# Optimization experiments

Measured on AMD Instinct MI355X. Metric: run time of the kernel, lower is better.

The kernel has to match this reference:

```python
import jax, jax.numpy as jnp
import numpy as np

N = 4096   # num_nodes
D_E = 16   # node embedding dim
H = 4      # heads
K = 3      # Chebyshev order
L = 64     # in_dim
B = 16     # batch


def setup_inputs() -> dict:
    key = jax.random.key(0)
    ks = jax.random.split(key, 8)
    return {
        "x": jax.random.normal(ks[0], (B, N, L), dtype=jnp.float32),
        "psi_emb": jax.random.normal(ks[1], (N, D_E), dtype=jnp.float32),
        "psi": jnp.asarray(1.0, dtype=jnp.float32),
        "W_q": jax.random.normal(ks[2], (D_E, H, D_E), dtype=jnp.float32),
        "W_k": jax.random.normal(ks[3], (D_E, H, D_E), dtype=jnp.float32),
        "attn_alpha": jnp.asarray(0.5, dtype=jnp.float32),
        "F_w": jax.random.normal(ks[4], (H, D_E, K + 1, L), dtype=jnp.float32),
        "f_b": jax.random.normal(ks[5], (H, D_E), dtype=jnp.float32),
        "head_mix": jnp.ones((H,), dtype=jnp.float32),
    }


def reference(x, psi_emb, psi, W_q, W_k, attn_alpha, F_w, f_b, head_mix):
    # x: (B, N, L) -> out: (B, N)
    Bx, Nx, Lx = x.shape

    # Gaussian adjacency: softmax over rows of exp(-psi * ||psi_i - psi_j||^2)
    diff = psi_emb[:, None, :] - psi_emb[None, :, :]      # (N, N, d_e)
    dist2 = jnp.sum(diff * diff, axis=-1)                 # (N, N)
    A_g = jax.nn.softmax(jnp.exp(-psi * dist2), axis=1)   # (N, N)

    # Per-head attention adjacency
    Q = jnp.einsum('nd,dhm->nhm', psi_emb, W_q)           # (N, H, d_e)
    Kt = jnp.einsum('nd,dhm->nhm', psi_emb, W_k)          # (N, H, d_e)
    scale = 1.0 / np.sqrt(Q.shape[-1]).astype(np.float32)
    attn = jnp.einsum('nhd,mhd->hnm', Q, Kt) * scale      # (H, N, N)
    A_attn = jax.nn.softmax(attn, axis=-1)

    # Sigmoid blend of gaussian and attention adjacencies
    alpha = jax.nn.sigmoid(attn_alpha)
    A_effs = alpha * A_g[None, :, :] + (1.0 - alpha) * A_attn  # (H, N, N)

    mix_w = jax.nn.softmax(head_mix)                      # (H,)
    I = jnp.eye(Nx, dtype=x.dtype)

    out = jnp.zeros((Bx, Nx), dtype=x.dtype)
    for h in range(H):  # small fixed head loop (structurally distinct params)
        A = A_effs[h]
        # Chebyshev recursion: T0=I, T1=A, Tk = 2 A T_{k-1} - T_{k-2}
        supports = [I, A]
        for _ in range(2, K + 1):
            supports.append(2.0 * (A @ supports[-1]) - supports[-2])
        S = jnp.stack(supports, axis=0)                   # (K+1, N, N)

        # Per-node filter weights / bias from node embeddings
        W_filter = jnp.einsum('nd,dkl->nkl', psi_emb, F_w[h])  # (N, K+1, L)
        b_filter = psi_emb @ f_b[h]                            # (N,)

        x_g = jnp.einsum('knm,bml->bknl', S, x)                # (B, K+1, N, L)
        out_h = jnp.einsum('bknl,nkl->bn', x_g, W_filter) + b_filter
        out = out + mix_w[h] * out_h
    return out
```

## Files before the change

kernel.cpp:

```cpp
#include <hip/hip_runtime.h>
#include <hip/hip_bf16.h>

#define NN 4096
#define DE 16
#define NH 4
#define LL 64
#define NB 16
#define CC 1024

typedef __attribute__((ext_vector_type(8))) short short8v;
typedef __attribute__((ext_vector_type(4))) float f32x4;

#define GLD_LDS16(gp, lp) __builtin_amdgcn_global_load_lds( \
    (const __attribute__((address_space(1))) unsigned int*)(gp), \
    (__attribute__((address_space(3))) unsigned int*)(lp), 16, 0, 0)

__device__ __forceinline__ unsigned short f2bf(float f){
  unsigned int u = __float_as_uint(f);
  u += 0x7fffu + ((u >> 16) & 1u);
  return (unsigned short)(u >> 16);
}
__device__ __forceinline__ float bf2f(unsigned short s){
  return __uint_as_float(((unsigned int)s) << 16);
}
__device__ __forceinline__ void get_mix(const float* hm, float* mw){
  float a=hm[0],b=hm[1],c=hm[2],d=hm[3];
  float m = fmaxf(fmaxf(a,b),fmaxf(c,d));
  float e0=__expf(a-m),e1=__expf(b-m),e2=__expf(c-m),e3=__expf(d-m);
  float inv = 1.0f/(e0+e1+e2+e3);
  mw[0]=e0*inv; mw[1]=e1*inv; mw[2]=e2*inv; mw[3]=e3*inv;
}

__global__ void k_prep(const float* __restrict__ psi_emb, const float* __restrict__ W_q,
                       const float* __restrict__ W_k, const float* __restrict__ f_b,
                       const float* __restrict__ head_mix,
                       unsigned short* __restrict__ Qh, unsigned short* __restrict__ Ql,
                       unsigned short* __restrict__ Kh, unsigned short* __restrict__ Kl,
                       unsigned short* __restrict__ Ph, unsigned short* __restrict__ Pl,
                       float* __restrict__ n2g, float* __restrict__ bias_comb){
  int n = blockIdx.x*blockDim.x + threadIdx.x;
  if (n >= NN) return;
  float p[DE];
  float n2 = 0.f;
  unsigned short ph[DE], pl[DE];
  #pragma unroll
  for (int d=0;d<DE;d++){
    p[d] = psi_emb[n*DE+d];
    n2 += p[d]*p[d];
    ph[d] = f2bf(p[d]);
    pl[d] = f2bf(p[d] - bf2f(ph[d]));
  }
  n2g[n] = n2;
  *(short8v*)(Ph + n*DE)     = *(short8v*)ph;
  *(short8v*)(Ph + n*DE + 8) = *(short8v*)(ph+8);
  *(short8v*)(Pl + n*DE)     = *(short8v*)pl;
  *(short8v*)(Pl + n*DE + 8) = *(short8v*)(pl+8);
  float mw[NH]; get_mix(head_mix, mw);
  float bias = 0.f;
  for (int h=0; h<NH; h++){
    unsigned short qh[DE], ql[DE], kh[DE], kl[DE];
    #pragma unroll
    for (int m=0;m<DE;m++){
      float q=0.f,k=0.f;
      #pragma unroll
      for (int d=0;d<DE;d++){
        q += p[d]*W_q[(d*NH+h)*DE+m];
        k += p[d]*W_k[(d*NH+h)*DE+m];
      }
      qh[m]=f2bf(q); ql[m]=f2bf(q - bf2f(qh[m]));
      kh[m]=f2bf(k); kl[m]=f2bf(k - bf2f(kh[m]));
    }
    size_t base = ((size_t)h*NN + n)*DE;
    *(short8v*)(Qh+base)=*(short8v*)qh;   *(short8v*)(Qh+base+8)=*(short8v*)(qh+8);
    *(short8v*)(Ql+base)=*(short8v*)ql;   *(short8v*)(Ql+base+8)=*(short8v*)(ql+8);
    *(short8v*)(Kh+base)=*(short8v*)kh;   *(short8v*)(Kh+base+8)=*(short8v*)(kh+8);
    *(short8v*)(Kl+base)=*(short8v*)kl;   *(short8v*)(Kl+base+8)=*(short8v*)(kl+8);
    float bh=0.f;
    #pragma unroll
    for (int d=0;d<DE;d++) bh += p[d]*f_b[h*DE+d];
    bias += mw[h]*bh;
  }
  bias_comb[n]=bias;
}

__global__ void k_wf(const float* __restrict__ psi_emb, const float* __restrict__ F_w,
                     const float* __restrict__ head_mix,
                     float* __restrict__ Wf_eff, float* __restrict__ W0c){
  int id = blockIdx.x*256 + threadIdx.x;
  int n = id & (NN-1);
  int kl = id >> 12;
  int l = kl & (LL-1);
  int k = kl >> 6;
  float mw[NH]; get_mix(head_mix, mw);
  float p[DE];
  #pragma unroll
  for (int d=0;d<DE;d++) p[d]=psi_emb[n*DE+d];
  float s0=0.f;
  for (int h=0;h<NH;h++){
    float v=0.f;
    #pragma unroll
    for (int d=0;d<DE;d++) v += p[d]*F_w[((h*DE+d)*4+k)*LL+l];
    v *= mw[h];
    Wf_eff[(((size_t)(h*4+k))*LL+l)*NN+n]=v;
    s0 += v;
  }
  if (k==0) W0c[(size_t)l*NN+n]=s0;
}

__global__ __launch_bounds__(256, 4) void k_adj(
    const unsigned short* __restrict__ Qh, const unsigned short* __restrict__ Ql,
    const unsigned short* __restrict__ Kh, const unsigned short* __restrict__ Kl,
    const unsigned short* __restrict__ Ph, const unsigned short* __restrict__ Pl,
    const float* __restrict__ n2g, const float* __restrict__ psi_p,
    const float* __restrict__ attn_alpha, unsigned short* __restrict__ A_all){
  __shared__ unsigned short T[4][16][72];
  __shared__ float st_g[4][16], st_m[4][16], st_s[4][16];
  __shared__ float fin_g[16], fin_m[16], fin_s[16];

  int tid = threadIdx.x;
  int lane = tid & 63, w = tid >> 6;
  int h = blockIdx.y;
  int n0 = blockIdx.x * 16;
  int kg = lane >> 4;
  int cl = lane & 15;
  float psi_v = psi_p[0];
  float alpha = 1.f/(1.f+__expf(-attn_alpha[0]));

  short8v z8 = {};
  int rown = n0 + cl;
  const unsigned short* qb = ((kg<2) ? Qh : Ql) + ((size_t)h*NN + rown)*DE + (kg&1)*8;
  const unsigned short* pb = ((kg<2) ? Ph : Pl) + (size_t)rown*DE + (kg&1)*8;
  short8v aF1 = *(const short8v*)qb;
  short8v gA1 = *(const short8v*)pb;
  short8v aF2 = z8, gA2 = z8;
  if (kg < 2){ aF2 = aF1; gA2 = gA1; }

  float n2row[4];
  #pragma unroll
  for (int r=0;r<4;r++) n2row[r] = n2g[n0 + kg*4 + r];

  float gsum[4], mx[4], sm[4];
  #pragma unroll
  for (int r=0;r<4;r++){ gsum[r]=0.f; mx[r]=-1e30f; sm[r]=0.f; }

  const size_t hN = (size_t)h*NN;
  int mbase = w * 1024;

  #pragma unroll 2
  for (int mt=0; mt<64; ++mt){
    int m0 = mbase + mt*16;
    int mm = m0 + cl;
    const unsigned short* kb = Kh + (hN + mm)*DE + (kg&1)*8;
    const unsigned short* pmb = Ph + (size_t)mm*DE + (kg&1)*8;
    short8v bF1 = *(const short8v*)kb;
    short8v gB1 = *(const short8v*)pmb;
    short8v bF2 = z8, gB2 = z8;
    if (kg < 2){
      bF2 = *(const short8v*)(Kl + (hN + mm)*DE + (kg&1)*8);
      gB2 = *(const short8v*)(Pl + (size_t)mm*DE + (kg&1)*8);
    }
    f32x4 zc = {};
    f32x4 sc = __builtin_amdgcn_mfma_f32_16x16x32_bf16(aF2, bF2, zc, 0,0,0);
    sc = __builtin_amdgcn_mfma_f32_16x16x32_bf16(aF1, bF1, sc, 0,0,0);
    f32x4 gc = __builtin_amdgcn_mfma_f32_16x16x32_bf16(gA2, gB2, zc, 0,0,0);
    gc = __builtin_amdgcn_mfma_f32_16x16x32_bf16(gA1, gB1, gc, 0,0,0);
    float n2m = n2g[m0 + cl];
    #pragma unroll
    for (int r=0;r<4;r++){
      float s = sc[r]*0.25f;
      float d2 = n2row[r] + n2m - 2.f*gc[r];
      float eg = __expf(__expf(-psi_v*d2));
      gsum[r] += eg;
      if (s > mx[r] + 8.f){
        sm[r] = sm[r]*__expf(mx[r]-s) + 1.f;
        mx[r] = s;
      } else {
        sm[r] += __expf(s - mx[r]);
      }
    }
  }
  #pragma unroll
  for (int off=1; off<16; off<<=1){
    #pragma unroll
    for (int r=0;r<4;r++){
      gsum[r] += __shfl_xor(gsum[r], off);
      float om = __shfl_xor(mx[r], off);
      float os = __shfl_xor(sm[r], off);
      float nm = fmaxf(mx[r], om);
      sm[r] = sm[r]*__expf(mx[r]-nm) + os*__expf(om-nm);
      mx[r] = nm;
    }
  }
  if (cl < 4){
    float g,m,s;
    if      (cl==0){ g=gsum[0]; m=mx[0]; s=sm[0]; }
    else if (cl==1){ g=gsum[1]; m=mx[1]; s=sm[1]; }
    else if (cl==2){ g=gsum[2]; m=mx[2]; s=sm[2]; }
    else           { g=gsum[3]; m=mx[3]; s=sm[3]; }
    int row = kg*4 + cl;
    st_g[w][row]=g; st_m[w][row]=m; st_s[w][row]=s;
  }
  __syncthreads();
  if (tid < 16){
    float G=0.f, M=-1e30f, S=0.f;
    #pragma unroll
    for (int ww=0; ww<4; ww++){
      G += st_g[ww][tid];
      float om = st_m[ww][tid], os = st_s[ww][tid];
      float nm = fmaxf(M, om);
      S = S*__expf(M-nm) + os*__expf(om-nm);
      M = nm;
    }
    fin_g[tid] = 1.f/G;
    fin_m[tid] = M;
    fin_s[tid] = 1.f/S;
  }
  __syncthreads();

  float fg[4], fm[4], fs[4];
  #pragma unroll
  for (int r=0;r<4;r++){
    fg[r]=fin_g[kg*4+r]; fm[r]=fin_m[kg*4+r]; fs[r]=fin_s[kg*4+r];
  }
  float a1 = alpha, a2 = 1.f - alpha;

  for (int mt=0; mt<64; ++mt){
    int m0 = mbase + mt*16;
    int mm = m0 + cl;
    const unsigned short* kb = Kh + (hN + mm)*DE + (kg&1)*8;
    const unsigned short* pmb = Ph + (size_t)mm*DE + (kg&1)*8;
    short8v bF1 = *(const short8v*)kb;
    short8v gB1 = *(const short8v*)pmb;
    short8v bF2 = z8, gB2 = z8;
    if (kg < 2){
      bF2 = *(const short8v*)(Kl + (hN + mm)*DE + (kg&1)*8);
      gB2 = *(const short8v*)(Pl + (size_t)mm*DE + (kg&1)*8);
    }
    f32x4 zc = {};
    f32x4 sc = __builtin_amdgcn_mfma_f32_16x16x32_bf16(aF2, bF2, zc, 0,0,0);
    sc = __builtin_amdgcn_mfma_f32_16x16x32_bf16(aF1, bF1, sc, 0,0,0);
    f32x4 gc = __builtin_amdgcn_mfma_f32_16x16x32_bf16(gA2, gB2, zc, 0,0,0);
    gc = __builtin_amdgcn_mfma_f32_16x16x32_bf16(gA1, gB1, gc, 0,0,0);
    float n2m = n2g[m0 + cl];
    #pragma unroll
    for (int r=0;r<4;r++){
      float s = sc[r]*0.25f;
      float d2 = n2row[r] + n2m - 2.f*gc[r];
      float eg = __expf(__expf(-psi_v*d2));
      float ag  = eg * fg[r];
      float aat = __expf(s - fm[r]) * fs[r];
      float a = a1*ag + a2*aat;
      T[w][kg*4+r][(mt&3)*16 + cl] = f2bf(a);
    }
    if ((mt & 3) == 3){
      int row = lane >> 2, cgp = lane & 3;
      short8v v0 = *(const short8v*)&T[w][row][cgp*16];
      short8v v1 = *(const short8v*)&T[w][row][cgp*16+8];
      unsigned short* dst = A_all + hN*NN + (size_t)(n0+row)*NN + mbase + (mt&~3)*16 + cgp*16;
      *(short8v*)dst = v0;
      *(short8v*)(dst+8) = v1;
    }
  }
}

__global__ __launch_bounds__(256) void k_xpose(const float* __restrict__ x,
                                               unsigned short* __restrict__ X){
  __shared__ float t[64][65];
  int b = blockIdx.y, n0 = blockIdx.x*64;
  int tid=threadIdx.x;
  int nr = tid>>2, lc=(tid&3)*16;
  const float* src = x + ((size_t)b*NN + n0 + nr)*LL + lc;
  #pragma unroll
  for (int j=0;j<16;j+=4){
    float4 v = *(const float4*)(src + j);
    t[nr][lc+j+0]=v.x; t[nr][lc+j+1]=v.y; t[nr][lc+j+2]=v.z; t[nr][lc+j+3]=v.w;
  }
  __syncthreads();
  int cl = tid>>2, mp=(tid&3)*16;
  short8v bufv[2];
  #pragma unroll
  for (int j=0;j<16;j++) bufv[j>>3][j&7] = (short)f2bf(t[mp+j][cl]);
  unsigned short* dst = X + (size_t)(b*LL+cl)*NN + n0 + mp;
  *(short8v*)dst = bufv[0];
  *(short8v*)(dst+8) = bufv[1];
}

__global__ void k_out0(const float* __restrict__ x, const float* __restrict__ W0c,
                       const float* __restrict__ bias_comb, float* __restrict__ out){
  int id = blockIdx.x*256+threadIdx.x;
  int n = id & (NN-1);
  float acc = bias_comb[n];
  const float* xp = x + (size_t)id*LL;
  #pragma unroll
  for (int l4=0;l4<LL;l4+=4){
    float4 xv = *(const float4*)(xp+l4);
    acc += xv.x*W0c[(size_t)(l4+0)*NN+n] + xv.y*W0c[(size_t)(l4+1)*NN+n]
         + xv.z*W0c[(size_t)(l4+2)*NN+n] + xv.w*W0c[(size_t)(l4+3)*NN+n];
  }
  out[id] = acc;
}

template<int HAS_PREV, int STORE>
__global__ __launch_bounds__(256) void k_cheb(
    const unsigned short* __restrict__ A_all,
    const unsigned short* __restrict__ Zin, size_t z_hs,
    const unsigned short* __restrict__ Yprev, size_t p_hs,
    unsigned short* __restrict__ Ynew, size_t y_hs,
    const float* __restrict__ Wf_eff, float* __restrict__ out,
    int kcheb, float scale)
{
  __shared__ unsigned short ZT[2][128][64];
  __shared__ unsigned short AT[2][128][64];
  int h = blockIdx.z;
  int n0 = blockIdx.x * 128;
  int c0 = blockIdx.y * 128;
  const unsigned short* Ah = A_all + (size_t)h*NN*NN;
  const unsigned short* Z  = Zin + z_hs*h;
  int tid = threadIdx.x;
  int lane = tid & 63, w = tid >> 6;
  int wr = w >> 1, wc = w & 1;
  f32x4 acc[4][4] = {};
  int lrow8 = lane >> 3;
  int scol  = ((lane & 7) ^ lrow8) * 8;
  const unsigned short* gA = Ah + (size_t)(n0 + w*32 + lrow8)*NN + scol;
  const unsigned short* gZ = Z  + (size_t)(c0 + w*32 + lrow8)*NN + scol;
  int frow = lane & 15;
  int rsw  = frow & 7;
  int fsl  = lane >> 4;

  #define STAGE(buf, m0) do { \
    _Pragma("unroll") \
    for (int jj = 0; jj < 4; ++jj) { \
      GLD_LDS16(gA + (size_t)(8*jj)*NN + (m0), &AT[buf][w*32 + 8*jj][0]); \
      GLD_LDS16(gZ + (size_t)(8*jj)*NN + (m0), &ZT[buf][w*32 + 8*jj][0]); \
    } \
  } while(0)

  STAGE(0, 0);

  for (int t = 0; t < 64; ++t) {
    int cur = t & 1;
    asm volatile("" ::: "memory");
    __builtin_amdgcn_s_barrier();
    __builtin_amdgcn_sched_barrier(0);
    if (t < 63) {
      STAGE(cur ^ 1, (t + 1) * 64);
      asm volatile("s_waitcnt vmcnt(8)" ::: "memory");
    } else {
      asm volatile("s_waitcnt vmcnt(0)" ::: "memory");
    }
    __builtin_amdgcn_s_barrier();
    __builtin_amdgcn_sched_barrier(0);
    #pragma unroll
    for (int kk = 0; kk < 64; kk += 32) {
      short8v af[4], bf[4];
      int sl = (((kk >> 3) + fsl) ^ rsw) * 8;
      #pragma unroll
      for (int i=0;i<4;i++) af[i] = *(const short8v*)&ZT[cur][wr*64 + i*16 + frow][sl];
      #pragma unroll
      for (int j=0;j<4;j++) bf[j] = *(const short8v*)&AT[cur][wc*64 + j*16 + frow][sl];
      #pragma unroll
      for (int i=0;i<4;i++)
        #pragma unroll
        for (int j=0;j<4;j++)
          acc[i][j] = __builtin_amdgcn_mfma_f32_16x16x32_bf16(af[i], bf[j], acc[i][j], 0, 0, 0);
    }
  }
  #undef STAGE

  int b = (c0 >> 6) + wr;
  int g4 = lane >> 4, nl = lane & 15;
  #pragma unroll
  for (int j=0;j<4;j++){
    int n = n0 + wc*64 + j*16 + nl;
    float psum = 0.f;
    #pragma unroll
    for (int i=0;i<4;i++){
      #pragma unroll
      for (int r=0;r<4;r++){
        int lx = i*16 + 4*g4 + r;
        size_t cn = (size_t)(b*64 + lx)*NN + n;
        float v = scale*acc[i][j][r];
        if (HAS_PREV) v -= bf2f(Yprev[p_hs*h + cn]);
        if (STORE) Ynew[y_hs*h + cn] = f2bf(v);
        psum += v * Wf_eff[(((size_t)(h*4 + kcheb))*LL + lx)*NN + n];
      }
    }
    psum += __shfl_xor(psum, 16);
    psum += __shfl_xor(psum, 32);
    if (g4 == 0) atomicAdd(out + (size_t)b*NN + n, psum);
  }
}

extern "C" void kernel_launch(void* const* d_in, const int* in_sizes, int n_in,
                              void* d_out, int out_size, void* d_ws, size_t ws_size,
                              hipStream_t stream) {
  const float* x         = (const float*)d_in[0];
  const float* psi_emb   = (const float*)d_in[1];
  const float* psi       = (const float*)d_in[2];
  const float* W_q       = (const float*)d_in[3];
  const float* W_k       = (const float*)d_in[4];
  const float* attn_alpha= (const float*)d_in[5];
  const float* F_w       = (const float*)d_in[6];
  const float* f_b       = (const float*)d_in[7];
  const float* head_mix  = (const float*)d_in[8];
  float* out = (float*)d_out;

  char* ws = (char*)d_ws;
  size_t off = 0;
  auto alloc = [&](size_t bytes)->void*{
    void* p = ws + off; off += (bytes + 255) & ~(size_t)255; return p;
  };
  unsigned short* A_all  = (unsigned short*)alloc((size_t)NH*NN*NN*2);
  unsigned short* X      = (unsigned short*)alloc((size_t)CC*NN*2);
  unsigned short* Y1     = (unsigned short*)alloc((size_t)NH*CC*NN*2);
  unsigned short* Y2     = (unsigned short*)alloc((size_t)NH*CC*NN*2);
  float* Wf_eff  = (float*)alloc((size_t)NH*4*LL*NN*4);
  float* W0c     = (float*)alloc((size_t)LL*NN*4);
  unsigned short* Qh = (unsigned short*)alloc((size_t)NH*NN*DE*2);
  unsigned short* Ql = (unsigned short*)alloc((size_t)NH*NN*DE*2);
  unsigned short* Kh = (unsigned short*)alloc((size_t)NH*NN*DE*2);
  unsigned short* Kl = (unsigned short*)alloc((size_t)NH*NN*DE*2);
  unsigned short* Ph = (unsigned short*)alloc((size_t)NN*DE*2);
  unsigned short* Pl = (unsigned short*)alloc((size_t)NN*DE*2);
  float* n2g     = (float*)alloc((size_t)NN*4);
  float* bias_c  = (float*)alloc((size_t)NN*4);

  k_prep<<<dim3(16), dim3(256), 0, stream>>>(psi_emb, W_q, W_k, f_b, head_mix,
                                             Qh, Ql, Kh, Kl, Ph, Pl, n2g, bias_c);
  k_wf<<<dim3(4096), dim3(256), 0, stream>>>(psi_emb, F_w, head_mix, Wf_eff, W0c);
  k_adj<<<dim3(256, NH), dim3(256), 0, stream>>>(Qh, Ql, Kh, Kl, Ph, Pl, n2g,
                                                 psi, attn_alpha, A_all);
  k_xpose<<<dim3(64, NB), dim3(256), 0, stream>>>(x, X);
  k_out0<<<dim3(256), dim3(256), 0, stream>>>(x, W0c, bias_c, out);

  dim3 gg(32, 8, NH);
  size_t CN = (size_t)CC*NN;
  k_cheb<0,1><<<gg, dim3(256), 0, stream>>>(A_all, X, (size_t)0, X, (size_t)0,
                                            Y1, CN, Wf_eff, out, 1, 1.0f);
  k_cheb<1,1><<<gg, dim3(256), 0, stream>>>(A_all, Y1, CN, X, (size_t)0,
                                            Y2, CN, Wf_eff, out, 2, 2.0f);
  k_cheb<1,0><<<gg, dim3(256), 0, stream>>>(A_all, Y2, CN, Y1, CN,
                                            Y2, (size_t)0, Wf_eff, out, 3, 2.0f);
  (void)in_sizes; (void)n_in; (void)out_size; (void)ws_size;
}
```

Measured before the change: 717.2 us.

## Enlarge Chebyshev GEMM tiles to 256x256 with 8 waves and interleaved staging

The Chebyshev propagation kernel moves from a 128x128 tile with 4 waves to a 256x256 tile with 8 waves. Each wave computes a 128x64 sub-tile, and LDS double buffers grow to 256 rows. The K-loop is split into four phases. Each phase issues a slice of the next tile's global-to-LDS loads between MFMA blocks, and the MFMA blocks are wrapped with barriers and s_setprio. The intent is more operand reuse per byte loaded and better overlap of memory with matrix math. The cost is a grid of only 256 blocks, more barriers per iteration, and higher register pressure from 32 accumulators.

```diff
diff --git a/kernel.cpp b/kernel.cpp
--- a/kernel.cpp
+++ b/kernel.cpp
@@ -301,7 +301,7 @@
 }
 
 template<int HAS_PREV, int STORE>
-__global__ __launch_bounds__(256) void k_cheb(
+__global__ __launch_bounds__(512, 2) void k_cheb(
     const unsigned short* __restrict__ A_all,
     const unsigned short* __restrict__ Zin, size_t z_hs,
     const unsigned short* __restrict__ Yprev, size_t p_hs,
@@ -309,86 +309,145 @@
     const float* __restrict__ Wf_eff, float* __restrict__ out,
     int kcheb, float scale)
 {
-  __shared__ unsigned short ZT[2][128][64];
-  __shared__ unsigned short AT[2][128][64];
+  __shared__ __align__(16) unsigned short ZT[2][256][64];
+  __shared__ __align__(16) unsigned short AT[2][256][64];
   int h = blockIdx.z;
-  int n0 = blockIdx.x * 128;
-  int c0 = blockIdx.y * 128;
+  int n0 = blockIdx.x * 256;
+  int c0 = blockIdx.y * 256;
   const unsigned short* Ah = A_all + (size_t)h*NN*NN;
   const unsigned short* Z  = Zin + z_hs*h;
   int tid = threadIdx.x;
   int lane = tid & 63, w = tid >> 6;
-  int wr = w >> 1, wc = w & 1;
-  f32x4 acc[4][4] = {};
-  int lrow8 = lane >> 3;
-  int scol  = ((lane & 7) ^ lrow8) * 8;
-  const unsigned short* gA = Ah + (size_t)(n0 + w*32 + lrow8)*NN + scol;
-  const unsigned short* gZ = Z  + (size_t)(c0 + w*32 + lrow8)*NN + scol;
-  int frow = lane & 15;
-  int rsw  = frow & 7;
-  int fsl  = lane >> 4;
-
-  #define STAGE(buf, m0) do { \
-    _Pragma("unroll") \
-    for (int jj = 0; jj < 4; ++jj) { \
-      GLD_LDS16(gA + (size_t)(8*jj)*NN + (m0), &AT[buf][w*32 + 8*jj][0]); \
-      GLD_LDS16(gZ + (size_t)(8*jj)*NN + (m0), &ZT[buf][w*32 + 8*jj][0]); \
-    } \
-  } while(0)
-
-  STAGE(0, 0);
+  int wr = w >> 2, wc = w & 3;
+  f32x4 acc[8][4] = {};
+
+  int ssc = ((lane & 7) ^ (lane >> 3)) * 8;
+  const unsigned short* gA0 = Ah + (size_t)(n0 + 8*w + (lane>>3))*NN + ssc;
+  const unsigned short* gZ0 = Z  + (size_t)(c0 + 8*w + (lane>>3))*NN + ssc;
+
+  int frow = lane & 15, fsl = lane >> 4;
+  int fx = frow & 7;
+  int s0 = ((0 + fsl) ^ fx) * 8;
+  int s1 = ((4 + fsl) ^ fx) * 8;
+
+#define SG_A(buf, q, m0n) GLD_LDS16(gA0 + (size_t)(64*(q))*NN + (m0n), &AT[buf][64*(q)+8*w][0])
+#define SG_Z(buf, q, m0n) GLD_LDS16(gZ0 + (size_t)(64*(q))*NN + (m0n), &ZT[buf][64*(q)+8*w][0])
+
+  SG_A(0,0,0); SG_A(0,1,0); SG_A(0,2,0); SG_A(0,3,0);
+  SG_Z(0,0,0); SG_Z(0,1,0); SG_Z(0,2,0); SG_Z(0,3,0);
 
   for (int t = 0; t < 64; ++t) {
     int cur = t & 1;
-    asm volatile("" ::: "memory");
-    __builtin_amdgcn_s_barrier();
-    __builtin_amdgcn_sched_barrier(0);
+    unsigned short (*zb)[64] = ZT[cur];
+    unsigned short (*ab)[64] = AT[cur];
+    int nm0 = (t+1)*64;
     if (t < 63) {
-      STAGE(cur ^ 1, (t + 1) * 64);
-      asm volatile("s_waitcnt vmcnt(8)" ::: "memory");
+      SG_A(cur^1, 0, nm0); SG_A(cur^1, 1, nm0);
+      asm volatile("s_waitcnt vmcnt(2)" ::: "memory");
     } else {
       asm volatile("s_waitcnt vmcnt(0)" ::: "memory");
     }
     __builtin_amdgcn_s_barrier();
     __builtin_amdgcn_sched_barrier(0);
-    #pragma unroll
-    for (int kk = 0; kk < 64; kk += 32) {
-      short8v af[4], bf[4];
-      int sl = (((kk >> 3) + fsl) ^ rsw) * 8;
+
+    short8v a4[4], b4[4];
+
+    #pragma unroll
+    for (int j=0;j<4;j++) b4[j] = *(const short8v*)&ab[wc*64 + j*16 + frow][s0];
+    #pragma unroll
+    for (int i=0;i<4;i++) a4[i] = *(const short8v*)&zb[wr*128 + i*16 + frow][s0];
+    __builtin_amdgcn_s_barrier();
+    asm volatile("s_waitcnt lgkmcnt(0)" ::: "memory");
+    __builtin_amdgcn_sched_barrier(0);
+    __builtin_amdgcn_s_setprio(1);
+    #pragma unroll
+    for (int i=0;i<4;i++)
       #pragma unroll
-      for (int i=0;i<4;i++) af[i] = *(const short8v*)&ZT[cur][wr*64 + i*16 + frow][sl];
+      for (int j=0;j<4;j++)
+        acc[i][j] = __builtin_amdgcn_mfma_f32_16x16x32_bf16(a4[i], b4[j], acc[i][j], 0,0,0);
+    __builtin_amdgcn_s_setprio(0);
+    __builtin_amdgcn_s_barrier();
+    __builtin_amdgcn_sched_barrier(0);
+
+    #pragma unroll
+    for (int i=0;i<4;i++) a4[i] = *(const short8v*)&zb[wr*128 + 64 + i*16 + frow][s0];
+    if (t < 63) { SG_A(cur^1, 2, nm0); SG_A(cur^1, 3, nm0); }
+    __builtin_amdgcn_s_barrier();
+    asm volatile("s_waitcnt lgkmcnt(0)" ::: "memory");
+    __builtin_amdgcn_sched_barrier(0);
+    __builtin_amdgcn_s_setprio(1);
+    #pragma unroll
+    for (int i=0;i<4;i++)
       #pragma unroll
-      for (int j=0;j<4;j++) bf[j] = *(const short8v*)&AT[cur][wc*64 + j*16 + frow][sl];
+      for (int j=0;j<4;j++)
+        acc[4+i][j] = __builtin_amdgcn_mfma_f32_16x16x32_bf16(a4[i], b4[j], acc[4+i][j], 0,0,0);
+    __builtin_amdgcn_s_setprio(0);
+    __builtin_amdgcn_s_barrier();
+    __builtin_amdgcn_sched_barrier(0);
+
+    #pragma unroll
+    for (int j=0;j<4;j++) b4[j] = *(const short8v*)&ab[wc*64 + j*16 + frow][s1];
+    #pragma unroll
+    for (int i=0;i<4;i++) a4[i] = *(const short8v*)&zb[wr*128 + i*16 + frow][s1];
+    if (t < 63) { SG_Z(cur^1, 0, nm0); SG_Z(cur^1, 1, nm0); }
+    __builtin_amdgcn_s_barrier();
+    asm volatile("s_waitcnt lgkmcnt(0)" ::: "memory");
+    __builtin_amdgcn_sched_barrier(0);
+    __builtin_amdgcn_s_setprio(1);
+    #pragma unroll
+    for (int i=0;i<4;i++)
       #pragma unroll
-      for (int i=0;i<4;i++)
+      for (int j=0;j<4;j++)
+        acc[i][j] = __builtin_amdgcn_mfma_f32_16x16x32_bf16(a4[i], b4[j], acc[i][j], 0,0,0);
+    __builtin_amdgcn_s_setprio(0);
+    __builtin_amdgcn_s_barrier();
+    __builtin_amdgcn_sched_barrier(0);
+
+    #pragma unroll
+    for (int i=0;i<4;i++) a4[i] = *(const short8v*)&zb[wr*128 + 64 + i*16 + frow][s1];
+    if (t < 63) { SG_Z(cur^1, 2, nm0); SG_Z(cur^1, 3, nm0); }
+    __builtin_amdgcn_s_barrier();
+    asm volatile("s_waitcnt lgkmcnt(0)" ::: "memory");
+    __builtin_amdgcn_sched_barrier(0);
+    __builtin_amdgcn_s_setprio(1);
+    #pragma unroll
+    for (int i=0;i<4;i++)
+      #pragma unroll
+      for (int j=0;j<4;j++)
+        acc[4+i][j] = __builtin_amdgcn_mfma_f32_16x16x32_bf16(a4[i], b4[j], acc[4+i][j], 0,0,0);
+    __builtin_amdgcn_s_setprio(0);
+    __builtin_amdgcn_s_barrier();
+    __builtin_amdgcn_sched_barrier(0);
+  }
+#undef SG_A
+#undef SG_Z
+
+  int g4 = lane >> 4, nl = lane & 15;
+  const float* wfb = Wf_eff + ((size_t)(h*4 + kcheb))*LL*NN;
+  #pragma unroll
+  for (int fn=0; fn<4; fn++){
+    int n = n0 + wc*64 + fn*16 + nl;
+    #pragma unroll
+    for (int bb=0; bb<2; bb++){
+      int bidx = (c0>>6) + wr*2 + bb;
+      float psum = 0.f;
+      #pragma unroll
+      for (int f4=0; f4<4; f4++){
+        int fm = bb*4 + f4;
         #pragma unroll
-        for (int j=0;j<4;j++)
-          acc[i][j] = __builtin_amdgcn_mfma_f32_16x16x32_bf16(af[i], bf[j], acc[i][j], 0, 0, 0);
-    }
-  }
-  #undef STAGE
-
-  int b = (c0 >> 6) + wr;
-  int g4 = lane >> 4, nl = lane & 15;
-  #pragma unroll
-  for (int j=0;j<4;j++){
-    int n = n0 + wc*64 + j*16 + nl;
-    float psum = 0.f;
-    #pragma unroll
-    for (int i=0;i<4;i++){
-      #pragma unroll
-      for (int r=0;r<4;r++){
-        int lx = i*16 + 4*g4 + r;
-        size_t cn = (size_t)(b*64 + lx)*NN + n;
-        float v = scale*acc[i][j][r];
-        if (HAS_PREV) v -= bf2f(Yprev[p_hs*h + cn]);
-        if (STORE) Ynew[y_hs*h + cn] = f2bf(v);
-        psum += v * Wf_eff[(((size_t)(h*4 + kcheb))*LL + lx)*NN + n];
+        for (int rr=0; rr<4; rr++){
+          int c = c0 + wr*128 + fm*16 + 4*g4 + rr;
+          size_t cn = (size_t)c*NN + n;
+          float v = scale*acc[fm][fn][rr];
+          if (HAS_PREV) v -= bf2f(Yprev[p_hs*h + cn]);
+          if (STORE) Ynew[y_hs*h + cn] = f2bf(v);
+          psum += v * wfb[(size_t)(c & 63)*NN + n];
+        }
       }
-    }
-    psum += __shfl_xor(psum, 16);
-    psum += __shfl_xor(psum, 32);
-    if (g4 == 0) atomicAdd(out + (size_t)b*NN + n, psum);
+      psum += __shfl_xor(psum, 16);
+      psum += __shfl_xor(psum, 32);
+      if (g4 == 0) atomicAdd(out + (size_t)bidx*NN + n, psum);
+    }
   }
 }
 
@@ -434,13 +493,13 @@
   k_xpose<<<dim3(64, NB), dim3(256), 0, stream>>>(x, X);
   k_out0<<<dim3(256), dim3(256), 0, stream>>>(x, W0c, bias_c, out);
 
-  dim3 gg(32, 8, NH);
+  dim3 gg(NN/256, CC/256, NH);
   size_t CN = (size_t)CC*NN;
-  k_cheb<0,1><<<gg, dim3(256), 0, stream>>>(A_all, X, (size_t)0, X, (size_t)0,
+  k_cheb<0,1><<<gg, dim3(512), 0, stream>>>(A_all, X, (size_t)0, X, (size_t)0,
                                             Y1, CN, Wf_eff, out, 1, 1.0f);
-  k_cheb<1,1><<<gg, dim3(256), 0, stream>>>(A_all, Y1, CN, X, (size_t)0,
+  k_cheb<1,1><<<gg, dim3(512), 0, stream>>>(A_all, Y1, CN, X, (size_t)0,
                                             Y2, CN, Wf_eff, out, 2, 2.0f);
-  k_cheb<1,0><<<gg, dim3(256), 0, stream>>>(A_all, Y2, CN, Y1, CN,
+  k_cheb<1,0><<<gg, dim3(512), 0, stream>>>(A_all, Y2, CN, Y1, CN,
                                             Y2, (size_t)0, Wf_eff, out, 3, 2.0f);
   (void)in_sizes; (void)n_in; (void)out_size; (void)ws_size;
 }
```

After: 765.5 us. 6.7% more time.
